# Kernel tuning notes

Measured on AMD Instinct MI355X. Metric: run time of the kernel, lower is better.

## Reference

```python
import jax, jax.numpy as jnp
import numpy as np

EMBED_DIM = 1024
NUM_HEADS = 16
HEAD_DIM = EMBED_DIM // NUM_HEADS
SCALE = HEAD_DIM ** -0.5


def setup_inputs() -> dict:
    key = jax.random.key(0)
    ks = jax.random.split(key, 5)
    B, N, D = 8, 1024, EMBED_DIM
    std = D ** -0.5
    x = jax.random.normal(ks[0], (B, N, D), dtype=jnp.float32)
    W_qkv = jax.random.normal(ks[1], (D, 3 * D), dtype=jnp.float32) * std
    b_qkv = jnp.zeros((3 * D,), dtype=jnp.float32)
    W_proj = jax.random.normal(ks[2], (D, D), dtype=jnp.float32) * std
    b_proj = jnp.zeros((D,), dtype=jnp.float32)
    return {"x": x, "W_qkv": W_qkv, "b_qkv": b_qkv, "W_proj": W_proj, "b_proj": b_proj}


def reference(x, W_qkv, b_qkv, W_proj, b_proj):
    B, N, D = x.shape
    H, hd = NUM_HEADS, HEAD_DIM
    # QKV projection: (B,N,3D) -> (3,B,H,N,hd)
    qkv = (x @ W_qkv + b_qkv).reshape(B, N, 3, H, hd).transpose(2, 0, 3, 1, 4)
    q, k, v = qkv[0], qkv[1], qkv[2]
    # scaled dot-product attention, full (B,H,N,N) scores as in original
    attn = jnp.einsum('bhqd,bhkd->bhqk', q, k) * SCALE
    attn = jax.nn.softmax(attn, axis=-1)
    out = jnp.einsum('bhqk,bhkd->bhqd', attn, v)  # (B,H,N,hd)
    out = out.transpose(0, 2, 1, 3).reshape(B, N, D)
    return out @ W_proj + b_proj
```

## Files before the change

kernel.cpp:

```cpp
#include <hip/hip_runtime.h>

#define AS1(p) ((const __attribute__((address_space(1))) void*)(p))
#define AS3(p) ((__attribute__((address_space(3))) void*)(p))

typedef __attribute__((ext_vector_type(8))) short bf16x8;
typedef __attribute__((ext_vector_type(4))) float f32x4;
typedef __attribute__((ext_vector_type(16))) float f32x16;

static constexpr int kBatch = 8;
static constexpr int kSeq = 1024;
static constexpr int kD = 1024;
static constexpr int kH = 16;
static constexpr int kHD = 64;
static constexpr int kRows = kBatch * kSeq;
static constexpr int kQKVCols = 3 * kD;

__device__ __forceinline__ unsigned short f2bf(float f) {
  union { float f; unsigned int u; } a; a.f = f;
  unsigned int r = a.u + 0x7fffu + ((a.u >> 16) & 1u);
  return (unsigned short)(r >> 16);
}

__device__ __forceinline__ unsigned pkbf(float a, float b) {
  unsigned r;
  asm("v_cvt_pk_bf16_f32 %0, %1, %2" : "=v"(r) : "v"(a), "v"(b));
  return r;
}

__device__ __forceinline__ int swap23(int x) {
  return (x & ~12) | ((x & 4) << 1) | ((x & 8) >> 1);
}

__global__ __launch_bounds__(256) void prep_kernel(
    const float* __restrict__ x, unsigned short* __restrict__ Xbf,
    const float* __restrict__ Wqkv, unsigned short* __restrict__ WqkvT,
    const float* __restrict__ Wproj, unsigned short* __restrict__ WpT) {
  const int bid = blockIdx.x, t = threadIdx.x;
  if (bid < 1024) {
    const int n4 = kRows * kD / 4;
    int i = bid * 256 + t;
    const int stride = 1024 * 256;
    for (; i < n4; i += stride) {
      float4 v = reinterpret_cast<const float4*>(x)[i];
      ushort4 o;
      o.x = f2bf(v.x); o.y = f2bf(v.y); o.z = f2bf(v.z); o.w = f2bf(v.w);
      reinterpret_cast<ushort4*>(Xbf)[i] = o;
    }
    return;
  }
  __shared__ float tile[32][33];
  const float* W; unsigned short* Wt; int cols, c0, r0;
  if (bid < 4096) {
    const int idx = bid - 1024;
    W = Wqkv; Wt = WqkvT; cols = kQKVCols;
    c0 = (idx % 96) * 32; r0 = (idx / 96) * 32;
  } else {
    const int idx = bid - 4096;
    W = Wproj; Wt = WpT; cols = kD;
    c0 = (idx % 32) * 32; r0 = (idx / 32) * 32;
  }
  const int tx = t & 31, ty = t >> 5;
#pragma unroll
  for (int i = 0; i < 32; i += 8)
    tile[ty + i][tx] = W[(size_t)(r0 + ty + i) * cols + (c0 + tx)];
  __syncthreads();
#pragma unroll
  for (int i = 0; i < 32; i += 8)
    Wt[(size_t)(c0 + ty + i) * 1024 + (r0 + tx)] = f2bf(tile[tx][ty + i]);
}

__global__ __launch_bounds__(256) void vtrans_kernel(
    const unsigned short* __restrict__ qkv, unsigned short* __restrict__ Vt) {
  __shared__ alignas(16) unsigned short tile[64][72];
  const int nt = blockIdx.x, bh = blockIdx.y;
  const int b = bh >> 4, h = bh & 15;
  const unsigned short* Vb = qkv + (size_t)b * kSeq * kQKVCols + 2 * kD + h * kHD;
  const int t = threadIdx.x;
#pragma unroll
  for (int r = 0; r < 2; ++r) {
    const int c = r * 256 + t;
    const int n = c >> 3, d8 = c & 7;
    uint4 v = *reinterpret_cast<const uint4*>(Vb + (size_t)(nt * 64 + n) * kQKVCols + d8 * 8);
    *reinterpret_cast<uint4*>(&tile[n][d8 * 8]) = v;
  }
  __syncthreads();
#pragma unroll
  for (int r = 0; r < 2; ++r) {
    const int c = r * 256 + t;
    const int d = c >> 3, n8 = c & 7;
    unsigned short w8[8];
#pragma unroll
    for (int j = 0; j < 8; ++j) w8[j] = tile[swap23(n8 * 8 + j)][d];
    *reinterpret_cast<uint4*>(Vt + (size_t)bh * kHD * kSeq + (size_t)d * kSeq + nt * 64 + n8 * 8) =
        *reinterpret_cast<uint4*>(w8);
  }
}

template <int MODE>
__global__ __launch_bounds__(256) void gemm_bt_kernel(
    const unsigned short* __restrict__ A,
    const unsigned short* __restrict__ Bt,
    const float* __restrict__ bias,
    void* __restrict__ Cout, unsigned short* __restrict__ Vt,
    int M, int Nn, int K) {
  constexpr int BK = 64;
  __shared__ alignas(16) unsigned short As[128 * BK];
  __shared__ alignas(16) unsigned short Bs[128 * BK];
  const int t = threadIdx.x;
  const int lane = t & 63;
  const int w = t >> 6;
  const int wr = w >> 1, wc = w & 1;
  const int l15 = lane & 15, lhi = lane >> 4;
  const int nwg = gridDim.x * gridDim.y;
  const int lin = blockIdx.y * gridDim.x + blockIdx.x;
  const int swz = (lin & 7) * (nwg >> 3) + (lin >> 3);
  const int row0 = (swz / gridDim.x) * 128;
  const int col0 = (swz % gridDim.x) * 128;

  f32x4 acc[4][4] = {};
  const int ldsb = (t & ~63) * 16;

  for (int k0 = 0; k0 < K; k0 += BK) {
    __syncthreads();
#pragma unroll
    for (int r = 0; r < 4; ++r) {
      int c = r * 256 + t;
      int arow = c >> 3;
      int ccol = ((c & 7) ^ (arow & 7)) * 8;
      const unsigned short* ga = A + (size_t)(row0 + arow) * K + (k0 + ccol);
      const unsigned short* gb = Bt + (size_t)(col0 + arow) * K + (k0 + ccol);
      char* la = (char*)As + r * 4096 + ldsb;
      char* lb = (char*)Bs + r * 4096 + ldsb;
      __builtin_amdgcn_global_load_lds(AS1(ga), AS3(la), 16, 0, 0);
      __builtin_amdgcn_global_load_lds(AS1(gb), AS3(lb), 16, 0, 0);
    }
    __syncthreads();
#pragma unroll
    for (int kk = 0; kk < 2; ++kk) {
      bf16x8 af[4], bfr[4];
#pragma unroll
      for (int mi = 0; mi < 4; ++mi) {
        int rowa = wr * 64 + mi * 16 + l15;
        int chunk = (kk * 4 + lhi) ^ (rowa & 7);
        af[mi] = *reinterpret_cast<const bf16x8*>((const char*)As + rowa * 128 + chunk * 16);
      }
#pragma unroll
      for (int ni = 0; ni < 4; ++ni) {
        int rowb = wc * 64 + ni * 16 + l15;
        int chunk = (kk * 4 + lhi) ^ (rowb & 7);
        bfr[ni] = *reinterpret_cast<const bf16x8*>((const char*)Bs + rowb * 128 + chunk * 16);
      }
#pragma unroll
      for (int mi = 0; mi < 4; ++mi)
#pragma unroll
        for (int ni = 0; ni < 4; ++ni)
          acc[mi][ni] = __builtin_amdgcn_mfma_f32_16x16x32_bf16(af[mi], bfr[ni], acc[mi][ni], 0, 0, 0);
    }
  }

  if (MODE == 3) {
#pragma unroll
    for (int mi = 0; mi < 4; ++mi) {
      const int rbase = row0 + wr * 64 + mi * 16 + lhi * 4;
      const int b = rbase >> 10, n = rbase & 1023;
      const int nbase = (n & ~63) | swap23(n & 63);
#pragma unroll
      for (int ni = 0; ni < 4; ++ni) {
        const int col = col0 + wc * 64 + ni * 16 + l15;
        const int hv = col >> 6;
        const int d = col & 63;
        const float bv = bias[col];
        uint2 uu;
        uu.x = pkbf(acc[mi][ni][0] + bv, acc[mi][ni][1] + bv);
        uu.y = pkbf(acc[mi][ni][2] + bv, acc[mi][ni][3] + bv);
        *reinterpret_cast<uint2*>(Vt + ((size_t)((b << 4) + hv) << 16) + d * 1024 + nbase) = uu;
      }
    }
    return;
  }

#pragma unroll
  for (int mi = 0; mi < 4; ++mi) {
    int rbase = row0 + wr * 64 + mi * 16 + lhi * 4;
#pragma unroll
    for (int ni = 0; ni < 4; ++ni) {
      int col = col0 + wc * 64 + ni * 16 + l15;
      float bv = bias[col];
#pragma unroll
      for (int j = 0; j < 4; ++j) {
        float v = acc[mi][ni][j] + bv;
        if (MODE != 0)
          ((unsigned short*)Cout)[(size_t)(rbase + j) * Nn + col] = f2bf(v);
        else
          ((float*)Cout)[(size_t)(rbase + j) * Nn + col] = v;
      }
    }
  }
}

#define G256_STAGE_A(BUF, HALF, KT)                                           \
  do {                                                                        \
    char* _d = smem + (BUF) * 65536 + (HALF) * 16384 + ldst;                  \
    const unsigned short* _s0 = Ap + aoff0 + (size_t)(HALF) * halfstep + (KT) * 64; \
    const unsigned short* _s1 = Ap + aoff1 + (size_t)(HALF) * halfstep + (KT) * 64; \
    __builtin_amdgcn_global_load_lds(AS1(_s0), AS3(_d), 16, 0, 0);            \
    __builtin_amdgcn_global_load_lds(AS1(_s1), AS3(_d + 8192), 16, 0, 0);     \
  } while (0)
#define G256_STAGE_B(BUF, HALF, KT)                                           \
  do {                                                                        \
    char* _d = smem + (BUF) * 65536 + 32768 + (HALF) * 16384 + ldst;          \
    const unsigned short* _s0 = Bp + boff0 + (size_t)(HALF) * halfstep + (KT) * 64; \
    const unsigned short* _s1 = Bp + boff1 + (size_t)(HALF) * halfstep + (KT) * 64; \
    __builtin_amdgcn_global_load_lds(AS1(_s0), AS3(_d), 16, 0, 0);            \
    __builtin_amdgcn_global_load_lds(AS1(_s1), AS3(_d + 8192), 16, 0, 0);     \
  } while (0)
#define G256_PHASE(RBUF, QM, QN, STAGE_STMT, DO_VM)                           \
  do {                                                                        \
    const char* _Ab = smem + (RBUF) * 65536 + (QM) * 16384;                   \
    const char* _Bb = smem + (RBUF) * 65536 + 32768 + (QN) * 16384;           \
    bf16x8 _af[2][4], _bf[2][2];                                              \
    _Pragma("unroll") for (int kk = 0; kk < 2; ++kk) {                        \
      _Pragma("unroll") for (int mi = 0; mi < 4; ++mi) {                      \
        const int rr = wm * 64 + mi * 16 + l15;                               \
        const int ch = (kk * 4 + lhi) ^ (rr & 7);                             \
        _af[kk][mi] = *reinterpret_cast<const bf16x8*>(_Ab + rr * 128 + ch * 16); \
      }                                                                       \
      _Pragma("unroll") for (int ni = 0; ni < 2; ++ni) {                      \
        const int rr = wn * 32 + ni * 16 + l15;                               \
        const int ch = (kk * 4 + lhi) ^ (rr & 7);                             \
        _bf[kk][ni] = *reinterpret_cast<const bf16x8*>(_Bb + rr * 128 + ch * 16); \
      }                                                                       \
    }                                                                         \
    STAGE_STMT;                                                               \
    if (DO_VM) asm volatile("s_waitcnt vmcnt(4)" ::: "memory");               \
    asm volatile("" ::: "memory");                                            \
    __builtin_amdgcn_s_barrier();                                             \
    asm volatile("s_waitcnt lgkmcnt(0)" ::: "memory");                        \
    __builtin_amdgcn_sched_barrier(0);                                        \
    __builtin_amdgcn_s_setprio(1);                                            \
    _Pragma("unroll") for (int kk = 0; kk < 2; ++kk)                          \
      _Pragma("unroll") for (int mi = 0; mi < 4; ++mi)                        \
        _Pragma("unroll") for (int ni = 0; ni < 2; ++ni)                      \
          acc[QM][QN][mi][ni] = __builtin_amdgcn_mfma_f32_16x16x32_bf16(      \
              _af[kk][mi], _bf[kk][ni], acc[QM][QN][mi][ni], 0, 0, 0);        \
    __builtin_amdgcn_s_setprio(0);                                            \
    asm volatile("" ::: "memory");                                            \
    __builtin_amdgcn_s_barrier();                                             \
    asm volatile("" ::: "memory");                                            \
  } while (0)

__global__ __launch_bounds__(512, 2) void gemm256_kernel(
    const unsigned short* __restrict__ Ap,
    const unsigned short* __restrict__ Bp,
    const float* __restrict__ bias,
    unsigned short* __restrict__ Cout, int M, int Nn, int K) {
  __shared__ alignas(16) char smem[131072];
  const int t = threadIdx.x;
  const int lane = t & 63;
  const int wid = t >> 6;
  const int wm = wid >> 2, wn = wid & 3;
  const int l15 = lane & 15, lhi = lane >> 4;

  const int nwg = gridDim.x * gridDim.y;
  const int lin = blockIdx.y * gridDim.x + blockIdx.x;
  const int swz = (lin & 7) * (nwg >> 3) + (lin >> 3);
  const int row0 = (swz / gridDim.x) * 256;
  const int col0 = (swz % gridDim.x) * 256;

  const int r0i = t >> 3, r1i = (512 + t) >> 3;
  const int sc0 = ((t & 7) ^ (r0i & 7)) * 8;
  const int sc1 = (((512 + t) & 7) ^ (r1i & 7)) * 8;
  const size_t aoff0 = (size_t)(row0 + r0i) * K + sc0;
  const size_t aoff1 = (size_t)(row0 + r1i) * K + sc1;
  const size_t boff0 = (size_t)(col0 + r0i) * K + sc0;
  const size_t boff1 = (size_t)(col0 + r1i) * K + sc1;
  const size_t halfstep = (size_t)128 * K;
  const int ldst = (t & ~63) * 16;

  f32x4 acc[2][2][4][2] = {};

  G256_STAGE_A(0, 0, 0);
  G256_STAGE_B(0, 1, 0);
  G256_STAGE_A(0, 1, 0);
  G256_STAGE_B(0, 0, 0);
  G256_STAGE_A(1, 0, 1);
  G256_STAGE_B(1, 1, 1);
  asm volatile("s_waitcnt vmcnt(4)" ::: "memory");
  __builtin_amdgcn_s_barrier();
  asm volatile("" ::: "memory");

  const int nkt = K >> 6;
  const int niter = nkt >> 1;
  for (int i = 0; i < niter; ++i) {
    const int tc1 = 2 * i + 1;
    const int tn0 = (2 * i + 2) & (nkt - 1);
    const int tn1 = (2 * i + 3) & (nkt - 1);
    G256_PHASE(0, 0, 0, G256_STAGE_A(1, 1, tc1), 0);
    G256_PHASE(0, 0, 1, G256_STAGE_B(1, 0, tc1), 0);
    G256_PHASE(0, 1, 1, G256_STAGE_A(0, 0, tn0), 0);
    G256_PHASE(0, 1, 0, G256_STAGE_B(0, 1, tn0), 1);
    G256_PHASE(1, 0, 0, G256_STAGE_A(0, 1, tn0), 0);
    G256_PHASE(1, 0, 1, G256_STAGE_B(0, 0, tn0), 0);
    G256_PHASE(1, 1, 1, G256_STAGE_A(1, 0, tn1), 0);
    G256_PHASE(1, 1, 0, G256_STAGE_B(1, 1, tn1), 1);
  }

#pragma unroll
  for (int qm = 0; qm < 2; ++qm)
#pragma unroll
    for (int mi = 0; mi < 4; ++mi) {
      const int rbase = row0 + qm * 128 + wm * 64 + mi * 16 + lhi * 4;
#pragma unroll
      for (int qn = 0; qn < 2; ++qn)
#pragma unroll
        for (int ni = 0; ni < 2; ++ni) {
          const int col = col0 + qn * 128 + wn * 32 + ni * 16 + l15;
          const float bv = bias[col];
#pragma unroll
          for (int j = 0; j < 4; ++j) {
            const float v = acc[qm][qn][mi][ni][j] + bv;
            Cout[(size_t)(rbase + j) * Nn + col] = f2bf(v);
          }
        }
    }
}

__global__ __launch_bounds__(256) void attn_kernel(
    const unsigned short* __restrict__ qkv,
    const unsigned short* __restrict__ Vt,
    unsigned short* __restrict__ ctx) {
  __shared__ alignas(16) char smem[32768];
  const int qt = blockIdx.x >> 7;
  const int bh = blockIdx.x & 127;
  const int b = bh >> 4, h = bh & 15;
  const int t = threadIdx.x, lane = t & 63, w = t >> 6;
  const int l31 = lane & 31, hi = lane >> 5;

  const unsigned short* Qb = qkv + (size_t)b * kSeq * kQKVCols + h * kHD;
  const unsigned short* Kb = Qb + kD;
  const unsigned short* Vtb = Vt + (size_t)bh * kHD * kSeq;

  bf16x8 qf[4];
  const int qrow = qt * 128 + w * 32 + l31;
#pragma unroll
  for (int s = 0; s < 4; ++s)
    qf[s] = *reinterpret_cast<const bf16x8*>(Qb + (size_t)qrow * kQKVCols + s * 16 + hi * 8);

  auto stage = [&](int kt, int bufb) {
#pragma unroll
    for (int r = 0; r < 2; ++r) {
      const int c = r * 256 + t;
      const int row = c >> 3;
      const int sc = ((c & 7) ^ (row & 7)) * 8;
      const unsigned short* gk = Kb + (size_t)(kt * 64 + row) * kQKVCols + sc;
      const unsigned short* gv = Vtb + (size_t)row * kSeq + kt * 64 + sc;
      char* lk = smem + bufb + r * 4096 + (t & ~63) * 16;
      char* lv = smem + bufb + 8192 + r * 4096 + (t & ~63) * 16;
      __builtin_amdgcn_global_load_lds(AS1(gk), AS3(lk), 16, 0, 0);
      __builtin_amdgcn_global_load_lds(AS1(gv), AS3(lv), 16, 0, 0);
    }
  };

  f32x16 oacc[2] = {};
  float mrun = -3.0e38f, lrun = 0.f;
  constexpr float kSc = 0.125f * 1.44269504f;

  stage(0, 0);
  __syncthreads();
  int cur = 0;
  for (int kt = 0; kt < 16; ++kt) {
    if (kt < 15) stage(kt + 1, (cur ^ 1) * 16384);
    const char* Kp = smem + cur * 16384;
    const char* Vp = Kp + 8192;

    f32x16 sacc[2] = {};
    __builtin_amdgcn_s_setprio(1);
#pragma unroll
    for (int nb = 0; nb < 2; ++nb) {
      const int n = nb * 32 + l31;
#pragma unroll
      for (int s = 0; s < 4; ++s) {
        const int ch = (s * 2 + hi) ^ (n & 7);
        bf16x8 kf = *reinterpret_cast<const bf16x8*>(Kp + n * 128 + ch * 16);
        sacc[nb] = __builtin_amdgcn_mfma_f32_32x32x16_bf16(kf, qf[s], sacc[nb], 0, 0, 0);
      }
    }
    __builtin_amdgcn_s_setprio(0);

    float tm = sacc[0][0];
#pragma unroll
    for (int nb = 0; nb < 2; ++nb)
#pragma unroll
      for (int r = 0; r < 16; ++r) tm = fmaxf(tm, sacc[nb][r]);
    tm = fmaxf(tm, __shfl_xor(tm, 32, 64));
    const float tms = tm * kSc;
    if (!__all(tms <= mrun + 8.0f)) {
      const float mnew = fmaxf(mrun, tms);
      const float corr = __builtin_amdgcn_exp2f(mrun - mnew);
      mrun = mnew;
      lrun *= corr;
#pragma unroll
      for (int db = 0; db < 2; ++db)
#pragma unroll
        for (int r = 0; r < 16; ++r) oacc[db][r] *= corr;
    }
    float ps = 0.f;
#pragma unroll
    for (int nb = 0; nb < 2; ++nb)
#pragma unroll
      for (int r = 0; r < 16; ++r) {
        const float e = __builtin_amdgcn_exp2f(__builtin_fmaf(sacc[nb][r], kSc, -mrun));
        sacc[nb][r] = e;
        ps += e;
      }
    lrun += ps + __shfl_xor(ps, 32, 64);

    bf16x8 pf[4];
#pragma unroll
    for (int s = 0; s < 4; ++s) {
      const int nb = s >> 1, h2 = (s & 1) * 8;
      union { unsigned u[4]; bf16x8 v; } pk4;
#pragma unroll
      for (int i = 0; i < 4; ++i)
        pk4.u[i] = pkbf(sacc[nb][h2 + 2 * i], sacc[nb][h2 + 2 * i + 1]);
      pf[s] = pk4.v;
    }

    __builtin_amdgcn_s_setprio(1);
#pragma unroll
    for (int db = 0; db < 2; ++db) {
      const int dr = db * 32 + l31;
#pragma unroll
      for (int s = 0; s < 4; ++s) {
        const int ch = (s * 2 + hi) ^ (dr & 7);
        bf16x8 vf = *reinterpret_cast<const bf16x8*>(Vp + dr * 128 + ch * 16);
        oacc[db] = __builtin_amdgcn_mfma_f32_32x32x16_bf16(vf, pf[s], oacc[db], 0, 0, 0);
      }
    }
    __builtin_amdgcn_s_setprio(0);
    __syncthreads();
    cur ^= 1;
  }

  const float rl = 1.0f / lrun;
  const int qlocal = w * 32 + l31;
#pragma unroll
  for (int db = 0; db < 2; ++db)
#pragma unroll
    for (int g = 0; g < 4; ++g) {
      const unsigned u0 = pkbf(oacc[db][g * 4 + 0] * rl, oacc[db][g * 4 + 1] * rl);
      const unsigned u1 = pkbf(oacc[db][g * 4 + 2] * rl, oacc[db][g * 4 + 3] * rl);
      const int ch = db * 4 + g;
      uint2 uu; uu.x = u0; uu.y = u1;
      *reinterpret_cast<uint2*>(smem + qlocal * 128 + ((ch ^ (qlocal & 7)) * 16) + hi * 8) = uu;
    }
  __syncthreads();
#pragma unroll
  for (int it = 0; it < 4; ++it) {
    const int idx = it * 256 + t;
    const int row = idx >> 3, ch = idx & 7;
    const uint4 vv = *reinterpret_cast<const uint4*>(smem + row * 128 + ((ch ^ (row & 7)) * 16));
    *reinterpret_cast<uint4*>(ctx + (size_t)(b * kSeq + qt * 128 + row) * kD + h * kHD + ch * 8) = vv;
  }
}

extern "C" void kernel_launch(void* const* d_in, const int* in_sizes, int n_in,
                              void* d_out, int out_size, void* d_ws, size_t ws_size,
                              hipStream_t stream) {
  const float* x     = (const float*)d_in[0];
  const float* Wqkv  = (const float*)d_in[1];
  const float* bqkv  = (const float*)d_in[2];
  const float* Wproj = (const float*)d_in[3];
  const float* bproj = (const float*)d_in[4];
  float* out = (float*)d_out;

  char* ws = (char*)d_ws;
  size_t oXbf   = 0;
  size_t oWqkvT = oXbf   + (size_t)kRows * kD * 2;
  size_t oWpT   = oWqkvT + (size_t)kQKVCols * kD * 2;
  size_t oQKV   = oWpT   + (size_t)kD * kD * 2;
  size_t oCTX   = oQKV   + (size_t)kRows * kQKVCols * 2;
  size_t oVt    = oCTX   + (size_t)kRows * kD * 2;
  size_t total_base  = oVt;
  size_t total_fused = oVt + (size_t)kRows * kD * 2;
  if (ws_size < total_base) return;
  const bool fused_vt = ws_size >= total_fused;

  unsigned short* Xbf   = (unsigned short*)(ws + oXbf);
  unsigned short* WqkvT = (unsigned short*)(ws + oWqkvT);
  unsigned short* WpT   = (unsigned short*)(ws + oWpT);
  unsigned short* QKV   = (unsigned short*)(ws + oQKV);
  unsigned short* CTX   = (unsigned short*)(ws + oCTX);
  unsigned short* VtF   = (unsigned short*)(ws + oVt);
  unsigned short* VtA   = (unsigned short*)(ws + oXbf);

  prep_kernel<<<5120, 256, 0, stream>>>(x, Xbf, Wqkv, WqkvT, Wproj, WpT);
  if (fused_vt) {
    gemm256_kernel<<<dim3(2048 / 256, kRows / 256), 512, 0, stream>>>(
        Xbf, WqkvT, bqkv, QKV, kRows, kQKVCols, kD);
    gemm_bt_kernel<3><<<dim3(1024 / 128, kRows / 128), 256, 0, stream>>>(
        Xbf, WqkvT + (size_t)2048 * kD, bqkv + 2048, nullptr, VtF,
        kRows, 1024, kD);
    attn_kernel<<<1024, 256, 0, stream>>>(QKV, VtF, CTX);
  } else {
    gemm_bt_kernel<1><<<dim3(kQKVCols / 128, kRows / 128), 256, 0, stream>>>(
        Xbf, WqkvT, bqkv, QKV, nullptr, kRows, kQKVCols, kD);
    vtrans_kernel<<<dim3(16, 128), 256, 0, stream>>>(QKV, VtA);
    attn_kernel<<<1024, 256, 0, stream>>>(QKV, VtA, CTX);
  }
  gemm_bt_kernel<0><<<dim3(kD / 128, kRows / 128), 256, 0, stream>>>(
      CTX, WpT, bproj, out, nullptr, kRows, kD, kD);
}
```

Before: 156.6 us.

## Pad attention LDS tiles, hoist staging pointers, use max3 and split row-sum

Pads the K/V shared-memory layout by 16 bytes per 8-row group (stride 1040 instead of 1024) to change bank mapping for the MFMA operand reads. Precomputes the global staging pointers once and advances them each tile instead of recomputing addresses. Replaces the serial max chain with a v_max3 tree and splits the exp row-sum into four accumulators to shorten dependency chains. LDS use grows slightly, and the summation order changes a little.

```diff
diff --git a/kernel.cpp b/kernel.cpp
--- a/kernel.cpp
+++ b/kernel.cpp
@@ -24,6 +24,12 @@
 __device__ __forceinline__ unsigned pkbf(float a, float b) {
   unsigned r;
   asm("v_cvt_pk_bf16_f32 %0, %1, %2" : "=v"(r) : "v"(a), "v"(b));
+  return r;
+}
+
+__device__ __forceinline__ float max3f(float a, float b, float c) {
+  float r;
+  asm("v_max3_f32 %0, %1, %2, %3" : "=v"(r) : "v"(a), "v"(b), "v"(c));
   return r;
 }
 
@@ -329,7 +335,7 @@
     const unsigned short* __restrict__ qkv,
     const unsigned short* __restrict__ Vt,
     unsigned short* __restrict__ ctx) {
-  __shared__ alignas(16) char smem[32768];
+  __shared__ alignas(16) char smem[33280];
   const int qt = blockIdx.x >> 7;
   const int bh = blockIdx.x & 127;
   const int b = bh >> 4, h = bh & 15;
@@ -346,18 +352,25 @@
   for (int s = 0; s < 4; ++s)
     qf[s] = *reinterpret_cast<const bf16x8*>(Qb + (size_t)qrow * kQKVCols + s * 16 + hi * 8);
 
-  auto stage = [&](int kt, int bufb) {
+  const int srow = t >> 3;
+  const int sc = ((t & 7) ^ (srow & 7)) * 8;
+  const unsigned short* gk[2];
+  const unsigned short* gv[2];
+#pragma unroll
+  for (int r = 0; r < 2; ++r) {
+    gk[r] = Kb + (size_t)(r * 32 + srow) * kQKVCols + sc;
+    gv[r] = Vtb + (size_t)(r * 32 + srow) * kSeq + sc;
+  }
+  const int wgrp = w * 1040;
+
+  auto stage = [&](int bufb) {
 #pragma unroll
     for (int r = 0; r < 2; ++r) {
-      const int c = r * 256 + t;
-      const int row = c >> 3;
-      const int sc = ((c & 7) ^ (row & 7)) * 8;
-      const unsigned short* gk = Kb + (size_t)(kt * 64 + row) * kQKVCols + sc;
-      const unsigned short* gv = Vtb + (size_t)row * kSeq + kt * 64 + sc;
-      char* lk = smem + bufb + r * 4096 + (t & ~63) * 16;
-      char* lv = smem + bufb + 8192 + r * 4096 + (t & ~63) * 16;
-      __builtin_amdgcn_global_load_lds(AS1(gk), AS3(lk), 16, 0, 0);
-      __builtin_amdgcn_global_load_lds(AS1(gv), AS3(lv), 16, 0, 0);
+      char* lk = smem + bufb + r * 4160 + wgrp;
+      __builtin_amdgcn_global_load_lds(AS1(gk[r]), AS3(lk), 16, 0, 0);
+      __builtin_amdgcn_global_load_lds(AS1(gv[r]), AS3(lk + 8320), 16, 0, 0);
+      gk[r] += 64 * kQKVCols;
+      gv[r] += 64;
     }
   };
 
@@ -365,33 +378,41 @@
   float mrun = -3.0e38f, lrun = 0.f;
   constexpr float kSc = 0.125f * 1.44269504f;
 
-  stage(0, 0);
+  stage(0);
   __syncthreads();
   int cur = 0;
+  const int rb7 = l31 & 7, rg = l31 >> 3;
   for (int kt = 0; kt < 16; ++kt) {
-    if (kt < 15) stage(kt + 1, (cur ^ 1) * 16384);
-    const char* Kp = smem + cur * 16384;
-    const char* Vp = Kp + 8192;
+    if (kt < 15) stage((cur ^ 1) * 16640);
+    const char* Kp = smem + cur * 16640;
+    const char* Vp = Kp + 8320;
 
     f32x16 sacc[2] = {};
     __builtin_amdgcn_s_setprio(1);
 #pragma unroll
     for (int nb = 0; nb < 2; ++nb) {
-      const int n = nb * 32 + l31;
+      const char* krow = Kp + (nb * 4 + rg) * 1040 + rb7 * 128;
 #pragma unroll
       for (int s = 0; s < 4; ++s) {
-        const int ch = (s * 2 + hi) ^ (n & 7);
-        bf16x8 kf = *reinterpret_cast<const bf16x8*>(Kp + n * 128 + ch * 16);
+        const int ch = (s * 2 + hi) ^ rb7;
+        bf16x8 kf = *reinterpret_cast<const bf16x8*>(krow + ch * 16);
         sacc[nb] = __builtin_amdgcn_mfma_f32_32x32x16_bf16(kf, qf[s], sacc[nb], 0, 0, 0);
       }
     }
     __builtin_amdgcn_s_setprio(0);
 
-    float tm = sacc[0][0];
-#pragma unroll
-    for (int nb = 0; nb < 2; ++nb)
-#pragma unroll
-      for (int r = 0; r < 16; ++r) tm = fmaxf(tm, sacc[nb][r]);
+    float vv[32];
+#pragma unroll
+    for (int r = 0; r < 16; ++r) { vv[r] = sacc[0][r]; vv[16 + r] = sacc[1][r]; }
+    float w1[11];
+#pragma unroll
+    for (int i = 0; i < 10; ++i) w1[i] = max3f(vv[3 * i], vv[3 * i + 1], vv[3 * i + 2]);
+    w1[10] = fmaxf(vv[30], vv[31]);
+    const float x0 = max3f(w1[0], w1[1], w1[2]);
+    const float x1 = max3f(w1[3], w1[4], w1[5]);
+    const float x2 = max3f(w1[6], w1[7], w1[8]);
+    const float x3 = fmaxf(w1[9], w1[10]);
+    float tm = fmaxf(max3f(x0, x1, x2), x3);
     tm = fmaxf(tm, __shfl_xor(tm, 32, 64));
     const float tms = tm * kSc;
     if (!__all(tms <= mrun + 8.0f)) {
@@ -404,15 +425,19 @@
 #pragma unroll
         for (int r = 0; r < 16; ++r) oacc[db][r] *= corr;
     }
-    float ps = 0.f;
+    float ps0 = 0.f, ps1 = 0.f, ps2 = 0.f, ps3 = 0.f;
 #pragma unroll
     for (int nb = 0; nb < 2; ++nb)
 #pragma unroll
       for (int r = 0; r < 16; ++r) {
         const float e = __builtin_amdgcn_exp2f(__builtin_fmaf(sacc[nb][r], kSc, -mrun));
         sacc[nb][r] = e;
-        ps += e;
-      }
+        if ((r & 3) == 0) ps0 += e;
+        else if ((r & 3) == 1) ps1 += e;
+        else if ((r & 3) == 2) ps2 += e;
+        else ps3 += e;
+      }
+    float ps = (ps0 + ps1) + (ps2 + ps3);
     lrun += ps + __shfl_xor(ps, 32, 64);
 
     bf16x8 pf[4];
@@ -429,11 +454,11 @@
     __builtin_amdgcn_s_setprio(1);
 #pragma unroll
     for (int db = 0; db < 2; ++db) {
-      const int dr = db * 32 + l31;
+      const char* vrow = Vp + (db * 4 + rg) * 1040 + rb7 * 128;
 #pragma unroll
       for (int s = 0; s < 4; ++s) {
-        const int ch = (s * 2 + hi) ^ (dr & 7);
-        bf16x8 vf = *reinterpret_cast<const bf16x8*>(Vp + dr * 128 + ch * 16);
+        const int ch = (s * 2 + hi) ^ rb7;
+        bf16x8 vf = *reinterpret_cast<const bf16x8*>(vrow + ch * 16);
         oacc[db] = __builtin_amdgcn_mfma_f32_32x32x16_bf16(vf, pf[s], oacc[db], 0, 0, 0);
       }
     }
```

After: 156.8 us. No clear change (+0.1%).
